# Kernel tuning notes

Hardware: AMD Instinct MI355X
Metric: run time of the kernel (lower is better)

Reference implementation:

```python
import jax, jax.numpy as jnp
import numpy as np

B, T, C = 4, 2048, 1024
H = 16
HD = C // H  # 64


def setup_inputs() -> dict:
    key = jax.random.key(0)
    k1, k2, k3 = jax.random.split(key, 3)
    x = jax.random.normal(k1, (B, T, C), dtype=jnp.float32)
    W_qkv = jax.random.normal(k2, (3 * C, C), dtype=jnp.float32) * (C ** -0.5)
    W_proj = jax.random.normal(k3, (C, C), dtype=jnp.float32) * (C ** -0.5)
    b_proj = jnp.zeros((C,), dtype=jnp.float32)
    return {"x": x, "W_qkv": W_qkv, "W_proj": W_proj, "b_proj": b_proj}


def reference(x, W_qkv, W_proj, b_proj):
    # qkv = x @ W_qkv.T : [B,T,3C]
    qkv = jnp.einsum('btc,oc->bto', x, W_qkv)
    # Faithful to torch: view(B,T,H,3*HD) then chunk last dim -> per-head q/k/v
    qkv = qkv.reshape(B, T, H, 3 * HD)
    q, k, v = jnp.split(qkv, 3, axis=-1)      # each [B,T,H,HD]
    q = q.transpose(0, 2, 1, 3)               # [B,H,T,HD]
    k = k.transpose(0, 2, 1, 3)
    v = v.transpose(0, 2, 1, 3)
    scale = HD ** -0.5
    att = jnp.einsum('bhqd,bhkd->bhqk', q, k) * scale  # [B,H,T,T]
    causal = jnp.tril(jnp.ones((T, T), dtype=bool))
    att = jnp.where(causal, att, -jnp.inf)
    att = jax.nn.softmax(att, axis=-1)
    out = jnp.einsum('bhqk,bhkd->bhqd', att, v)        # [B,H,T,HD]
    out = out.transpose(0, 2, 1, 3).reshape(B, T, C)
    out = jnp.einsum('btc,oc->bto', out, W_proj) + b_proj
    return out
```

## Files before the change

kernel.cpp:

```cpp
#include <hip/hip_runtime.h>
#include <stdint.h>

#define B_ 4
#define T_ 2048
#define C_ 1024
#define H_ 16
#define HD_ 64

typedef __attribute__((ext_vector_type(8))) short short8;
typedef __attribute__((ext_vector_type(4))) float f32x4;

typedef uint32_t __attribute__((address_space(3))) lds_u32;
typedef const uint32_t __attribute__((address_space(1))) glb_u32;

__device__ inline void async16(const void* g, void* l) {
    __builtin_amdgcn_global_load_lds((glb_u32*)g, (lds_u32*)l, 16, 0, 0);
}

__device__ inline short f2bf(float f) {
    union { float f; uint32_t u; } x; x.f = f;
    uint32_t r = (x.u + 0x7fffu + ((x.u >> 16) & 1u)) >> 16;
    return (short)r;
}
__device__ inline float bf2f(short b) {
    union { uint32_t u; float f; } x; x.u = ((uint32_t)(uint16_t)b) << 16;
    return x.f;
}
__device__ inline uint32_t cvt_pk_bf16(float lo, float hi) {
    uint32_t r;
    asm("v_cvt_pk_bf16_f32 %0, %1, %2" : "=v"(r) : "v"(lo), "v"(hi));
    return r;
}

#define FENCE asm volatile("" ::: "memory")
#define BAR   do { FENCE; __builtin_amdgcn_s_barrier(); FENCE; } while (0)
#define VMC6  asm volatile("s_waitcnt vmcnt(6)" ::: "memory")

__global__ void convert_all(const void* __restrict__ x,  const void* __restrict__ wq,
                            const void* __restrict__ wp, const void* __restrict__ bias,
                            short* __restrict__ xd, short* __restrict__ wqd,
                            short* __restrict__ wpd, short* __restrict__ biasd,
                            int* __restrict__ flag_out)
{
    __shared__ int cnt;
    if (threadIdx.x == 0) cnt = 0;
    __syncthreads();
    int sane = 0;
    const uint32_t* xu = (const uint32_t*)x;
    for (int i = threadIdx.x; i < 1024; i += 256) {
        float v = bf2f((short)(xu[i] & 0xFFFFu));
        float a = fabsf(v);
        if (a > 1e-5f && a < 1e5f) sane++;
    }
    atomicAdd(&cnt, sane);
    __syncthreads();
    const int isf32 = (cnt < 512) ? 1 : 0;

    const int blk = blockIdx.x;
    if (blk == 6144 && threadIdx.x == 0) *flag_out = isf32;
    if (!isf32) return;

    const void* src; short* dst; int base, n;
    if (blk < 4096)      { src = x;    dst = xd;    base = blk;        n = B_*T_*C_; }
    else if (blk < 5632) { src = wq;   dst = wqd;   base = blk - 4096; n = 3*C_*C_; }
    else if (blk < 6144) { src = wp;   dst = wpd;   base = blk - 5632; n = C_*C_; }
    else                 { src = bias; dst = biasd; base = 0;          n = C_; }
    const int i = (base * 256 + threadIdx.x) * 8;
    if (i >= n) return;
    const float* s = (const float*)src;
    short8 o;
#pragma unroll
    for (int j = 0; j < 8; j++) o[j] = f2bf(s[i + j]);
    *(short8*)&dst[i] = o;
}

template <bool DUAL>
__global__ __launch_bounds__(512, 2) void gemm8(
    const short* __restrict__ Abf,  const short* __restrict__ Araw,
    const short* __restrict__ Bbf,  const short* __restrict__ Braw,
    const short* __restrict__ biasbf, const short* __restrict__ biasraw,
    void* __restrict__ Cout, int M, int N, int K, const int* __restrict__ flag)
{
    __shared__ short lds[73728];
    const int isf32 = *flag;
    const short* __restrict__ A  = isf32 ? Abf : Araw;
    const short* __restrict__ Bm = isf32 ? Bbf : Braw;
    const short* bias_bf = DUAL ? (isf32 ? biasbf : biasraw) : (const short*)0;

    const int tid  = threadIdx.x;
    const int lane = tid & 63;
    const int wid  = tid >> 6;
    const int quad = lane >> 4;
    const int lcol = lane & 15;
    const int wm   = wid >> 2;
    const int wn   = wid & 3;
    const int nbx  = N >> 8;

    const int cpx = gridDim.x >> 3;
    const int wg  = (blockIdx.x & 7) * cpx + (blockIdx.x >> 3);
    const int m0 = (wg / nbx) << 7;
    const int n0 = (wg % nbx) << 8;

    const int srow = tid >> 3;
    const int sch  = ((tid & 7) ^ (srow & 7)) << 3;
    auto stA = [&](int buf, int i, int kt) {
        async16(&A[(size_t)(m0 + i * 64 + srow) * K + kt * 64 + sch],
                &lds[buf * 8192 + i * 4096 + tid * 8]);
    };
    auto stB = [&](int buf, int i, int kt) {
        async16(&Bm[(size_t)(n0 + i * 64 + srow) * K + kt * 64 + sch],
                &lds[24576 + buf * 16384 + i * 4096 + tid * 8]);
    };
    auto stage6 = [&](int buf, int kt) {
        stB(buf, 0, kt); stB(buf, 1, kt); stB(buf, 2, kt); stB(buf, 3, kt);
        stA(buf, 0, kt); stA(buf, 1, kt);
    };

    f32x4 acc[4][4];
#pragma unroll
    for (int i = 0; i < 4; i++)
#pragma unroll
        for (int j = 0; j < 4; j++) acc[i][j] = f32x4{0.f, 0.f, 0.f, 0.f};

    short8 a[4][2], b[4][2];
    auto rdA2 = [&](int mb, int buf) {
#pragma unroll
        for (int m2 = 0; m2 < 2; m2++)
#pragma unroll
            for (int ks = 0; ks < 2; ks++)
                a[mb + m2][ks] = *(const short8*)&lds[buf * 8192
                    + (wm * 64 + (mb + m2) * 16 + lcol) * 64
                    + ((((ks << 2) | quad) ^ (lcol & 7)) << 3)];
    };
    auto rdB2 = [&](int nb, int buf) {
#pragma unroll
        for (int n2 = 0; n2 < 2; n2++)
#pragma unroll
            for (int ks = 0; ks < 2; ks++)
                b[nb + n2][ks] = *(const short8*)&lds[24576 + buf * 16384
                    + (wn * 64 + (nb + n2) * 16 + lcol) * 64
                    + ((((ks << 2) | quad) ^ (lcol & 7)) << 3)];
    };
    auto mmq = [&](int mb, int nb) {
#pragma unroll
        for (int m2 = 0; m2 < 2; m2++)
#pragma unroll
            for (int n2 = 0; n2 < 2; n2++)
#pragma unroll
                for (int ks = 0; ks < 2; ks++)
                    acc[mb + m2][nb + n2] = __builtin_amdgcn_mfma_f32_16x16x32_bf16(
                        a[mb + m2][ks], b[nb + n2][ks], acc[mb + m2][nb + n2], 0, 0, 0);
    };

    const int NT = K >> 6;
    stage6(0, 0);
    stage6(1, 1);

    int bt = 0, b1i = 1, b2i = 2;
    for (int t = 0; t < NT; ++t) {
        const int ts = (t + 2 < NT) ? t + 2 : NT - 1;
        VMC6;
        BAR;
        rdA2(0, bt); rdA2(2, bt); rdB2(0, bt); rdB2(2, bt);
        stage6(b2i, ts);
        __builtin_amdgcn_s_setprio(1);
        mmq(0, 0); mmq(2, 0); mmq(0, 2); mmq(2, 2);
        __builtin_amdgcn_s_setprio(0);
        const int nb = bt;
        bt = b1i; b1i = b2i; b2i = nb;
    }

    float bv[4];
#pragma unroll
    for (int nf = 0; nf < 4; nf++)
        bv[nf] = bias_bf ? bf2f(bias_bf[n0 + wn * 64 + nf * 16 + lcol]) : 0.f;
#pragma unroll
    for (int mf = 0; mf < 4; mf++)
#pragma unroll
        for (int r = 0; r < 4; r++) {
            const int row = m0 + wm * 64 + mf * 16 + quad * 4 + r;
#pragma unroll
            for (int nf = 0; nf < 4; nf++) {
                const int col = n0 + wn * 64 + nf * 16 + lcol;
                const float val = acc[mf][nf][r] + bv[nf];
                const size_t off = (size_t)row * N + col;
                if (DUAL && isf32) ((float*)Cout)[off] = val;
                else               ((short*)Cout)[off] = f2bf(val);
            }
        }
}

__global__ __launch_bounds__(256) void attn(const short* __restrict__ qkv,
                                            short* __restrict__ att)
{
    __shared__ short lds_k[64][72];
    __shared__ short lds_vt[64][68];

    const int tid  = threadIdx.x;
    const int lane = tid & 63;
    const int wave = tid >> 6;
    const int quad = lane >> 4;
    const int lcol = lane & 15;

    const int bh   = blockIdx.x & 63;
    const int j    = blockIdx.x >> 6;
    const int b    = bh >> 4;
    const int h    = bh & 15;

    const size_t rowstride = 3 * C_;
    const size_t bhbase = (size_t)b * T_ * rowstride + (size_t)h * (3 * HD_);

    const int kkey = tid >> 2;
    const int kdp  = (tid & 3) * 16;
    const int vkey = tid & 63;
    const int vkp  = (vkey & 0x23) | ((vkey & 0x0C) << 1) | ((vkey & 0x10) >> 2);
    const int vd0  = (tid >> 6) * 16;

    short8 vones;
#pragma unroll
    for (int i = 0; i < 8; i++) vones[i] = (short)0x3F80;

    const short* kp; const short* vp;
    short8 kA, kB, vA, vB;
    const size_t TILE_STEP = (size_t)64 * rowstride;
    auto load_init = [&]() {
        kp = &qkv[bhbase + (size_t)kkey * rowstride + HD_ + kdp];
        vp = &qkv[bhbase + (size_t)vkey * rowstride + 2 * HD_ + vd0];
    };
    auto load_tile = [&]() {
        kA = *(const short8*)kp;
        kB = *(const short8*)(kp + 8);
        vA = *(const short8*)vp;
        vB = *(const short8*)(vp + 8);
        kp += TILE_STEP; vp += TILE_STEP;
    };

    const float SC = 0.1803368801f;
    auto scale_frag = [&](short8 q) {
        short8 r;
#pragma unroll
        for (int i = 0; i < 8; i++) r[i] = f2bf(bf2f(q[i]) * SC);
        return r;
    };

    auto process_chunk = [&](int qblk, bool sync_first) {
        const int q0 = qblk * 128;
        const int qA = q0 + wave * 16;
        const int qB = q0 + 64 + wave * 16;

        short8 qfA0, qfA1, qfB0, qfB1;
        {
            const size_t ba = bhbase + (size_t)(qA + lcol) * rowstride + quad * 8;
            qfA0 = scale_frag(*(const short8*)&qkv[ba]);
            qfA1 = scale_frag(*(const short8*)&qkv[ba + 32]);
            const size_t bb = bhbase + (size_t)(qB + lcol) * rowstride + quad * 8;
            qfB0 = scale_frag(*(const short8*)&qkv[bb]);
            qfB1 = scale_frag(*(const short8*)&qkv[bb + 32]);
        }

        f32x4 oA[4], oB[4], oLA, oLB;
#pragma unroll
        for (int i = 0; i < 4; i++) { oA[i] = f32x4{0.f,0.f,0.f,0.f}; oB[i] = f32x4{0.f,0.f,0.f,0.f}; }
        oLA = f32x4{0.f,0.f,0.f,0.f}; oLB = f32x4{0.f,0.f,0.f,0.f};

        load_init();
        load_tile();

        const int LT = 2 * qblk + 1;
        for (int kt = 0; kt <= LT; ++kt) {
            if (kt || sync_first) __syncthreads();
            *(short8*)&lds_k[kkey][kdp]     = kA;
            *(short8*)&lds_k[kkey][kdp + 8] = kB;
#pragma unroll
            for (int jj = 0; jj < 8; jj++) {
                lds_vt[vd0 + jj][vkp]     = vA[jj];
                lds_vt[vd0 + 8 + jj][vkp] = vB[jj];
            }
            __syncthreads();
            if (kt < LT) load_tile();

            const int k0 = kt * 64;
            const bool doA = (kt < LT);

            f32x4 SA[4], SB[4];
#pragma unroll
            for (int t = 0; t < 4; t++) {
                const short8 kf0 = *(const short8*)&lds_k[t * 16 + lcol][quad * 8];
                const short8 kf1 = *(const short8*)&lds_k[t * 16 + lcol][32 + quad * 8];
                SB[t] = f32x4{0.f, 0.f, 0.f, 0.f};
                SB[t] = __builtin_amdgcn_mfma_f32_16x16x32_bf16(kf0, qfB0, SB[t], 0, 0, 0);
                SB[t] = __builtin_amdgcn_mfma_f32_16x16x32_bf16(kf1, qfB1, SB[t], 0, 0, 0);
                if (doA) {
                    SA[t] = f32x4{0.f, 0.f, 0.f, 0.f};
                    SA[t] = __builtin_amdgcn_mfma_f32_16x16x32_bf16(kf0, qfA0, SA[t], 0, 0, 0);
                    SA[t] = __builtin_amdgcn_mfma_f32_16x16x32_bf16(kf1, qfA1, SA[t], 0, 0, 0);
                }
            }

            short8 vf[4][2];
#pragma unroll
            for (int dt = 0; dt < 4; dt++) {
                vf[dt][0] = *(const short8*)&lds_vt[dt * 16 + lcol][quad * 8];
                vf[dt][1] = *(const short8*)&lds_vt[dt * 16 + lcol][32 + quad * 8];
            }

            auto do_mtile = [&](f32x4 (&S)[4], f32x4 (&o)[4], f32x4& oL,
                                int qX, bool maskT) {
                if (maskT) {
                    const int qthr = qX + lcol - k0 - quad * 4;
#pragma unroll
                    for (int t = 0; t < 4; t++)
#pragma unroll
                        for (int r = 0; r < 4; r++) {
                            float e = __builtin_amdgcn_exp2f(S[t][r]);
                            if (t * 16 + r > qthr) e = 0.f;
                            S[t][r] = e;
                        }
                } else {
#pragma unroll
                    for (int t = 0; t < 4; t++)
#pragma unroll
                        for (int r = 0; r < 4; r++)
                            S[t][r] = __builtin_amdgcn_exp2f(S[t][r]);
                }
                union { uint32_t u[4]; short8 s; } p0, p1;
#pragma unroll
                for (int w = 0; w < 4; w++) {
                    const int t0 = w >> 1, r0 = (w & 1) * 2;
                    p0.u[w] = cvt_pk_bf16(S[t0][r0],     S[t0][r0 + 1]);
                    p1.u[w] = cvt_pk_bf16(S[2 + t0][r0], S[2 + t0][r0 + 1]);
                }
                oL = __builtin_amdgcn_mfma_f32_16x16x32_bf16(p0.s, vones, oL, 0, 0, 0);
                oL = __builtin_amdgcn_mfma_f32_16x16x32_bf16(p1.s, vones, oL, 0, 0, 0);
#pragma unroll
                for (int dt = 0; dt < 4; dt++) {
                    o[dt] = __builtin_amdgcn_mfma_f32_16x16x32_bf16(p0.s, vf[dt][0], o[dt], 0, 0, 0);
                    o[dt] = __builtin_amdgcn_mfma_f32_16x16x32_bf16(p1.s, vf[dt][1], o[dt], 0, 0, 0);
                }
            };

            if (doA) do_mtile(SA, oA, oLA, qA, kt == LT - 1);
            do_mtile(SB, oB, oLB, qB, kt == LT);
        }

#pragma unroll
        for (int r = 0; r < 4; r++) {
            const float la = oLA[r], lb = oLB[r];
            const float iar = (la > 0.f) ? 1.f / la : 0.f;
            const float ibr = (lb > 0.f) ? 1.f / lb : 0.f;
            const int qi  = quad * 4 + r;
            const int qrA = qA + qi;
            const int qrB = qB + qi;
#pragma unroll
            for (int dt = 0; dt < 4; dt++) {
                const int col = h * HD_ + dt * 16 + lcol;
                att[(size_t)(b * T_ + qrA) * C_ + col] = f2bf(oA[dt][r] * iar);
                att[(size_t)(b * T_ + qrB) * C_ + col] = f2bf(oB[dt][r] * ibr);
            }
        }
    };

    process_chunk(15 - j, false);
    process_chunk(j, true);
}

extern "C" void kernel_launch(void* const* d_in, const int* in_sizes, int n_in,
                              void* d_out, int out_size, void* d_ws, size_t ws_size,
                              hipStream_t stream) {
    char* ws = (char*)d_ws;
    short* qkv     = (short*)(ws);
    short* x_or_at = (short*)(ws + 50331648);
    short* wq_bf   = (short*)(ws + 50331648 + 16777216);
    short* wp_bf   = (short*)(ws + 50331648 + 16777216 + 6291456);
    short* bias_bf = (short*)(ws + 50331648 + 16777216 + 6291456 + 2097152);
    int*   flag    = (int*)  (ws + 50331648 + 16777216 + 6291456 + 2097152 + 2048);

    const short* x_raw    = (const short*)d_in[0];
    const short* wq_raw   = (const short*)d_in[1];
    const short* wp_raw   = (const short*)d_in[2];
    const short* bias_raw = (const short*)d_in[3];

    dim3 blk(256);

    convert_all<<<dim3(6145), blk, 0, stream>>>(
        d_in[0], d_in[1], d_in[2], d_in[3],
        x_or_at, wq_bf, wp_bf, bias_bf, flag);

    gemm8<false><<<dim3(768), dim3(512), 0, stream>>>(
        x_or_at, x_raw, wq_bf, wq_raw, nullptr, nullptr,
        qkv, B_ * T_, 3 * C_, C_, flag);

    attn<<<dim3(B_ * H_ * (T_ / 256)), blk, 0, stream>>>(qkv, x_or_at);

    gemm8<true><<<dim3(256), dim3(512), 0, stream>>>(
        x_or_at, x_or_at, wp_bf, wp_raw, bias_bf, bias_raw,
        d_out, B_ * T_, C_, C_, flag);
}
```

Measured before the change: 236.3 us.

## Load GEMM B-operand fragments directly from global into registers, bypassing LDS

The B tile is no longer staged through LDS with async global-to-LDS copies. Each wave now loads its own B fragments straight from global memory into double-buffered registers, two k-steps ahead, while A stays in a 3-stage LDS ring. This cuts the LDS footprint from 144KB to 48KB and removes the LDS reads for B. The wait count is raised to match the extra outstanding loads. The cost is uncoalesced 16-byte global loads, more register pressure, and B being reloaded by each of the two M-waves that share it. The loop now also assumes NT is even.

```diff
diff --git a/kernel.cpp b/kernel.cpp
--- a/kernel.cpp
+++ b/kernel.cpp
@@ -34,7 +34,7 @@
 
 #define FENCE asm volatile("" ::: "memory")
 #define BAR   do { FENCE; __builtin_amdgcn_s_barrier(); FENCE; } while (0)
-#define VMC6  asm volatile("s_waitcnt vmcnt(6)" ::: "memory")
+#define VMC10 asm volatile("s_waitcnt vmcnt(10)" ::: "memory")
 
 __global__ void convert_all(const void* __restrict__ x,  const void* __restrict__ wq,
                             const void* __restrict__ wp, const void* __restrict__ bias,
@@ -81,7 +81,7 @@
     const short* __restrict__ biasbf, const short* __restrict__ biasraw,
     void* __restrict__ Cout, int M, int N, int K, const int* __restrict__ flag)
 {
-    __shared__ short lds[73728];
+    __shared__ short lds[24576];
     const int isf32 = *flag;
     const short* __restrict__ A  = isf32 ? Abf : Araw;
     const short* __restrict__ Bm = isf32 ? Bbf : Braw;
@@ -103,17 +103,21 @@
 
     const int srow = tid >> 3;
     const int sch  = ((tid & 7) ^ (srow & 7)) << 3;
-    auto stA = [&](int buf, int i, int kt) {
-        async16(&A[(size_t)(m0 + i * 64 + srow) * K + kt * 64 + sch],
-                &lds[buf * 8192 + i * 4096 + tid * 8]);
-    };
-    auto stB = [&](int buf, int i, int kt) {
-        async16(&Bm[(size_t)(n0 + i * 64 + srow) * K + kt * 64 + sch],
-                &lds[24576 + buf * 16384 + i * 4096 + tid * 8]);
-    };
-    auto stage6 = [&](int buf, int kt) {
-        stB(buf, 0, kt); stB(buf, 1, kt); stB(buf, 2, kt); stB(buf, 3, kt);
-        stA(buf, 0, kt); stA(buf, 1, kt);
+    auto stage2A = [&](int buf, int kt) {
+        async16(&A[(size_t)(m0 + srow) * K + kt * 64 + sch],
+                &lds[buf * 8192 + tid * 8]);
+        async16(&A[(size_t)(m0 + 64 + srow) * K + kt * 64 + sch],
+                &lds[buf * 8192 + 4096 + tid * 8]);
+    };
+
+    const short* bbase = &Bm[(size_t)(n0 + wn * 64 + lcol) * K + quad * 8];
+    auto loadB = [&](short8 (&bb)[4][2], int kt) {
+        const short* p = bbase + kt * 64;
+#pragma unroll
+        for (int nb = 0; nb < 4; nb++)
+#pragma unroll
+            for (int ks = 0; ks < 2; ks++)
+                bb[nb][ks] = *(const short8*)(p + (size_t)nb * 16 * K + ks * 32);
     };
 
     f32x4 acc[4][4];
@@ -122,7 +126,7 @@
 #pragma unroll
         for (int j = 0; j < 4; j++) acc[i][j] = f32x4{0.f, 0.f, 0.f, 0.f};
 
-    short8 a[4][2], b[4][2];
+    short8 a[4][2];
     auto rdA2 = [&](int mb, int buf) {
 #pragma unroll
         for (int m2 = 0; m2 < 2; m2++)
@@ -132,16 +136,7 @@
                     + (wm * 64 + (mb + m2) * 16 + lcol) * 64
                     + ((((ks << 2) | quad) ^ (lcol & 7)) << 3)];
     };
-    auto rdB2 = [&](int nb, int buf) {
-#pragma unroll
-        for (int n2 = 0; n2 < 2; n2++)
-#pragma unroll
-            for (int ks = 0; ks < 2; ks++)
-                b[nb + n2][ks] = *(const short8*)&lds[24576 + buf * 16384
-                    + (wn * 64 + (nb + n2) * 16 + lcol) * 64
-                    + ((((ks << 2) | quad) ^ (lcol & 7)) << 3)];
-    };
-    auto mmq = [&](int mb, int nb) {
+    auto mmq = [&](short8 (&bb)[4][2], int mb, int nb) {
 #pragma unroll
         for (int m2 = 0; m2 < 2; m2++)
 #pragma unroll
@@ -149,25 +144,32 @@
 #pragma unroll
                 for (int ks = 0; ks < 2; ks++)
                     acc[mb + m2][nb + n2] = __builtin_amdgcn_mfma_f32_16x16x32_bf16(
-                        a[mb + m2][ks], b[nb + n2][ks], acc[mb + m2][nb + n2], 0, 0, 0);
+                        a[mb + m2][ks], bb[nb + n2][ks], acc[mb + m2][nb + n2], 0, 0, 0);
     };
 
     const int NT = K >> 6;
-    stage6(0, 0);
-    stage6(1, 1);
+    short8 bb0[4][2], bb1[4][2];
+
+    stage2A(0, 0); loadB(bb0, 0);
+    stage2A(1, 1); loadB(bb1, 1);
 
     int bt = 0, b1i = 1, b2i = 2;
-    for (int t = 0; t < NT; ++t) {
+    auto iter = [&](short8 (&bb)[4][2], int t) {
         const int ts = (t + 2 < NT) ? t + 2 : NT - 1;
-        VMC6;
+        VMC10;
         BAR;
-        rdA2(0, bt); rdA2(2, bt); rdB2(0, bt); rdB2(2, bt);
-        stage6(b2i, ts);
+        rdA2(0, bt); rdA2(2, bt);
+        stage2A(b2i, ts);
         __builtin_amdgcn_s_setprio(1);
-        mmq(0, 0); mmq(2, 0); mmq(0, 2); mmq(2, 2);
+        mmq(bb, 0, 0); mmq(bb, 2, 0); mmq(bb, 0, 2); mmq(bb, 2, 2);
         __builtin_amdgcn_s_setprio(0);
-        const int nb = bt;
-        bt = b1i; b1i = b2i; b2i = nb;
+        loadB(bb, ts);
+        const int nb2 = bt; bt = b1i; b1i = b2i; b2i = nb2;
+    };
+
+    for (int i = 0; i < NT / 2; i++) {
+        iter(bb0, 2 * i);
+        iter(bb1, 2 * i + 1);
     }
 
     float bv[4];
```

New measurement: 323.2 us. +36.7%, slower.
